# Kernel optimization log

Hardware: AMD Instinct MI355X
Metric: run time of the kernel (lower is better)

The kernel has to match this reference:

```python
import jax, jax.numpy as jnp
import numpy as np

D_MODEL = 1024
HEADS = 16
DILATION = 4
LN_EPS = 1e-5


def setup_inputs() -> dict:
    key = jax.random.key(0)
    ks = jax.random.split(key, 11)
    B, S, D = 2, 4096, D_MODEL
    x = jax.random.normal(ks[0], (B, S, D), dtype=jnp.float32)
    def lin(k):
        kw, kb = jax.random.split(k)
        W = jax.random.normal(kw, (D, D), dtype=jnp.float32) * 0.02  # torch Linear layout [out, in]
        b = jax.random.normal(kb, (D,), dtype=jnp.float32) * 0.02
        return W, b
    Wq, bq = lin(ks[1])
    Wk, bk = lin(ks[2])
    Wv, bv = lin(ks[3])
    Wf, bf = lin(ks[4])
    gamma = jnp.ones((D,), dtype=jnp.float32)
    beta = jnp.zeros((D,), dtype=jnp.float32)
    return {"x": x, "Wq": Wq, "bq": bq, "Wk": Wk, "bk": bk,
            "Wv": Wv, "bv": bv, "Wf": Wf, "bf": bf,
            "gamma": gamma, "beta": beta}


def _layer_norm(x, gamma, beta):
    mu = jnp.mean(x, axis=-1, keepdims=True)
    var = jnp.mean(jnp.square(x - mu), axis=-1, keepdims=True)
    return (x - mu) * jax.lax.rsqrt(var + LN_EPS) * gamma + beta


def reference(x, Wq, bq, Wk, bk, Wv, bv, Wf, bf, gamma, beta):
    B, S, D = x.shape
    dil, H = DILATION, HEADS
    dh = D // H
    pad = (-S) % dil  # padding_size
    xp = jnp.pad(x, ((0, 0), (0, pad), (0, 0)))
    Sp = S + pad
    L = Sp // dil
    # strided (atrous) regrouping: [B, Sp, D] -> [B*dil, L, D]
    xr = xp.reshape(B, L, dil, D).transpose(0, 2, 1, 3).reshape(B * dil, L, D)
    q = xr @ Wq.T + bq
    k = xr @ Wk.T + bk
    v = xr @ Wv.T + bv
    # split heads: [B*dil, H, L, dh]
    q = q.reshape(B * dil, L, H, dh).transpose(0, 2, 1, 3)
    k = k.reshape(B * dil, L, H, dh).transpose(0, 2, 1, 3)
    v = v.reshape(B * dil, L, H, dh).transpose(0, 2, 1, 3)
    scores = jnp.einsum('bhqd,bhkd->bhqk', q, k) / jnp.sqrt(jnp.float32(dh))
    probs = jax.nn.softmax(scores, axis=-1)
    ctx = jnp.einsum('bhqk,bhkd->bhqd', probs, v)
    # merge heads and undo atrous regrouping
    ctx = ctx.transpose(0, 2, 1, 3).reshape(B * dil, L, D)
    ctx = ctx.reshape(B, dil, L, D).transpose(0, 2, 1, 3).reshape(B, Sp, D)
    ctx = ctx[:, :S]
    atted = ctx @ Wf.T + bf  # dropout p=0.0
    final = _layer_norm(atted + x, gamma, beta)
    return (final, atted)
```

## Files before the change

### kernel.cpp

```cpp
#include <hip/hip_runtime.h>
#include <cstdint>
#include <cstddef>

constexpr int B_  = 2;
constexpr int S_  = 4096;
constexpr int D_  = 1024;
constexpr int H_  = 16;
constexpr int DH_ = 64;
constexpr int DIL = 4;
constexpr int L_  = S_ / DIL;
constexpr int M_  = B_ * S_;

typedef __attribute__((ext_vector_type(8))) short short8;
typedef __attribute__((ext_vector_type(4))) float f32x4;

__device__ __forceinline__ unsigned short f2b(float f) {
    union { float f; unsigned u; } v;
    v.f = f;
    unsigned r = v.u + 0x7fff + ((v.u >> 16) & 1);
    return (unsigned short)(r >> 16);
}

#define GLOAD16(gptr, lptr)                                                    \
    __builtin_amdgcn_global_load_lds(                                          \
        (const __attribute__((address_space(1))) void*)(gptr),                 \
        (__attribute__((address_space(3))) void*)(lptr), 16, 0, 0)

__global__ __launch_bounds__(256)
void conv_f2b(const float* __restrict__ in, unsigned short* __restrict__ out, int n4) {
    int i = blockIdx.x * 256 + threadIdx.x;
    if (i < n4) {
        float4 v = reinterpret_cast<const float4*>(in)[i];
        ushort4 o;
        o.x = f2b(v.x); o.y = f2b(v.y); o.z = f2b(v.z); o.w = f2b(v.w);
        reinterpret_cast<ushort4*>(out)[i] = o;
    }
}

template <int OUT_BF16>
__global__ __launch_bounds__(256)
void gemm_mfma(const unsigned short* __restrict__ A,
               const unsigned short* __restrict__ W,
               const float* __restrict__ bias,
               void* __restrict__ Cout, int M, int N, int K) {
    __shared__ unsigned short As[128 * 64];
    __shared__ unsigned short Bs[128 * 64];

    const int tid  = threadIdx.x;
    const int lane = tid & 63, wave = tid >> 6;
    const int l15 = lane & 15, l4 = lane >> 4;
    const int wr = wave >> 1, wc = wave & 1;
    const int bm = blockIdx.y * 128, bn = blockIdx.x * 128;

    f32x4 acc[4][4] = {};

    for (int k0 = 0; k0 < K; k0 += 64) {
        #pragma unroll
        for (int i = 0; i < 4; ++i) {
            int ch = i * 256 + wave * 64 + lane;
            int r = ch >> 3, c8 = ch & 7;
            const unsigned short* ga = A + (size_t)(bm + r) * K + k0 + c8 * 8;
            GLOAD16(ga, (char*)As + (size_t)(i * 256 + wave * 64) * 16);
            const unsigned short* gb = W + (size_t)(bn + r) * K + k0 + c8 * 8;
            GLOAD16(gb, (char*)Bs + (size_t)(i * 256 + wave * 64) * 16);
        }
        __syncthreads();

        #pragma unroll
        for (int ks = 0; ks < 2; ++ks) {
            short8 af[4], bf[4];
            #pragma unroll
            for (int mi = 0; mi < 4; ++mi)
                af[mi] = *reinterpret_cast<const short8*>(
                    &As[(wr * 64 + mi * 16 + l15) * 64 + ks * 32 + l4 * 8]);
            #pragma unroll
            for (int ni = 0; ni < 4; ++ni)
                bf[ni] = *reinterpret_cast<const short8*>(
                    &Bs[(wc * 64 + ni * 16 + l15) * 64 + ks * 32 + l4 * 8]);
            #pragma unroll
            for (int mi = 0; mi < 4; ++mi)
                #pragma unroll
                for (int ni = 0; ni < 4; ++ni)
                    acc[mi][ni] = __builtin_amdgcn_mfma_f32_16x16x32_bf16(
                        af[mi], bf[ni], acc[mi][ni], 0, 0, 0);
        }
        __syncthreads();
    }

    #pragma unroll
    for (int ni = 0; ni < 4; ++ni) {
        int col = bn + wc * 64 + ni * 16 + l15;
        float bv = bias[col];
        #pragma unroll
        for (int mi = 0; mi < 4; ++mi) {
            #pragma unroll
            for (int r = 0; r < 4; ++r) {
                int row = bm + wr * 64 + mi * 16 + l4 * 4 + r;
                float v = acc[mi][ni][r] + bv;
                if (OUT_BF16)
                    ((unsigned short*)Cout)[(size_t)row * N + col] = f2b(v);
                else
                    ((float*)Cout)[(size_t)row * N + col] = v;
            }
        }
    }
}

__global__ __launch_bounds__(256)
void gemm_qkv(const unsigned short* __restrict__ A,
              const unsigned short* __restrict__ W,
              const float* __restrict__ bq, const float* __restrict__ bk,
              const float* __restrict__ bv,
              unsigned short* __restrict__ Qb, unsigned short* __restrict__ Kb,
              unsigned short* __restrict__ Vb, int M, int K) {
    __shared__ unsigned short As[128 * 64];
    __shared__ unsigned short Bs[128 * 64];

    const int tid  = threadIdx.x;
    const int lane = tid & 63, wave = tid >> 6;
    const int l15 = lane & 15, l4 = lane >> 4;
    const int wr = wave >> 1, wc = wave & 1;
    const int bm = blockIdx.y * 128, bn = blockIdx.x * 128;

    f32x4 acc[4][4] = {};

    for (int k0 = 0; k0 < K; k0 += 64) {
        #pragma unroll
        for (int i = 0; i < 4; ++i) {
            int ch = i * 256 + wave * 64 + lane;
            int r = ch >> 3, c8 = ch & 7;
            const unsigned short* ga = A + (size_t)(bm + r) * K + k0 + c8 * 8;
            GLOAD16(ga, (char*)As + (size_t)(i * 256 + wave * 64) * 16);
            const unsigned short* gb = W + (size_t)(bn + r) * K + k0 + c8 * 8;
            GLOAD16(gb, (char*)Bs + (size_t)(i * 256 + wave * 64) * 16);
        }
        __syncthreads();

        #pragma unroll
        for (int ks = 0; ks < 2; ++ks) {
            short8 af[4], bf[4];
            #pragma unroll
            for (int mi = 0; mi < 4; ++mi)
                af[mi] = *reinterpret_cast<const short8*>(
                    &As[(wr * 64 + mi * 16 + l15) * 64 + ks * 32 + l4 * 8]);
            #pragma unroll
            for (int ni = 0; ni < 4; ++ni)
                bf[ni] = *reinterpret_cast<const short8*>(
                    &Bs[(wc * 64 + ni * 16 + l15) * 64 + ks * 32 + l4 * 8]);
            #pragma unroll
            for (int mi = 0; mi < 4; ++mi)
                #pragma unroll
                for (int ni = 0; ni < 4; ++ni)
                    acc[mi][ni] = __builtin_amdgcn_mfma_f32_16x16x32_bf16(
                        af[mi], bf[ni], acc[mi][ni], 0, 0, 0);
        }
        __syncthreads();
    }

    const int seg = bn >> 10;
    const float* bp = (seg == 0) ? bq : (seg == 1) ? bk : bv;
    unsigned short* ob = (seg == 0) ? Qb : (seg == 1) ? Kb : Vb;
    const int cb = bn & 1023;

    #pragma unroll
    for (int ni = 0; ni < 4; ++ni) {
        int col = cb + wc * 64 + ni * 16 + l15;
        float bvv = bp[col];
        #pragma unroll
        for (int mi = 0; mi < 4; ++mi) {
            #pragma unroll
            for (int r = 0; r < 4; ++r) {
                int row = bm + wr * 64 + mi * 16 + l4 * 4 + r;
                ob[(size_t)row * 1024 + col] = f2b(acc[mi][ni][r] + bvv);
            }
        }
    }
}

__global__ __launch_bounds__(256)
void attn_mfma(const unsigned short* __restrict__ Q,
               const unsigned short* __restrict__ K,
               const unsigned short* __restrict__ V,
               unsigned short* __restrict__ O) {
    __shared__ unsigned short Ks[2][64 * 64];
    __shared__ unsigned short Vt[2][64 * 64];

    const int tid = threadIdx.x;
    const int lane = tid & 63, wave = tid >> 6;
    const int l15 = lane & 15, l4 = lane >> 4;
    const int blk = blockIdx.x;
    const int qt = blk & 15;
    const int h  = (blk >> 4) & 15;
    const int bd = blk >> 8;
    const int b = bd >> 2, dd = bd & 3;
    const size_t rowbase = (size_t)b * S_;
    const int colbase = h * DH_;

    short8 qf[2];
    {
        int q = qt * 64 + wave * 16 + l15;
        const unsigned short* qp =
            Q + (rowbase + (size_t)q * DIL + dd) * D_ + colbase;
        qf[0] = *reinterpret_cast<const short8*>(qp + l4 * 8);
        qf[1] = *reinterpret_cast<const short8*>(qp + 32 + l4 * 8);
    }

    auto stageK = [&](int kt, int buf) {
        #pragma unroll
        for (int i = 0; i < 2; ++i) {
            int key = i * 32 + wave * 8 + (lane >> 3);
            int srcc = (lane & 7) ^ (lane >> 3);
            const unsigned short* g =
                K + (rowbase + (size_t)(kt * 64 + key) * DIL + dd) * D_ + colbase + srcc * 8;
            GLOAD16(g, (char*)&Ks[buf][0] + (size_t)(i * 256 + wave * 64) * 16);
        }
    };
    auto loadV = [&](int kt, int i) {
        int c8 = wave * 2 + i;
        return *reinterpret_cast<const short8*>(
            V + (rowbase + (size_t)(kt * 64 + lane) * DIL + dd) * D_ + colbase + c8 * 8);
    };
    auto writeV = [&](int buf, short8 va, short8 vb) {
        #pragma unroll
        for (int i = 0; i < 2; ++i) {
            short8 v = i ? vb : va;
            int c8 = wave * 2 + i;
            #pragma unroll
            for (int j = 0; j < 8; ++j)
                Vt[buf][(c8 * 8 + j) * 64 + (((lane >> 3) ^ j) * 8) + (lane & 7)] =
                    (unsigned short)v[j];
        }
    };

    f32x4 oT[4] = {};
    float m_run = -1e30f, l_run = 0.f;

    stageK(0, 0);
    {
        short8 va = loadV(0, 0), vb = loadV(0, 1);
        writeV(0, va, vb);
    }
    __syncthreads();

    const int srcA = ((l4 & 1) * 2) * 16 + l15;
    const int srcB = srcA + 16;
    const bool hi = (l4 & 2) != 0;

    for (int kt = 0; kt < L_ / 64; ++kt) {
        int cur = kt & 1, nxt = cur ^ 1;
        short8 va, vb;
        if (kt < L_ / 64 - 1) {
            stageK(kt + 1, nxt);
            va = loadV(kt + 1, 0);
            vb = loadV(kt + 1, 1);
        }

        f32x4 sT[4];
        #pragma unroll
        for (int n = 0; n < 4; ++n) {
            int row = n * 16 + l15;
            short8 kf0 = *reinterpret_cast<const short8*>(
                &Ks[cur][row * 64 + ((0 * 4 + l4) ^ (l15 & 7)) * 8]);
            short8 kf1 = *reinterpret_cast<const short8*>(
                &Ks[cur][row * 64 + ((1 * 4 + l4) ^ (l15 & 7)) * 8]);
            f32x4 z = {0.f, 0.f, 0.f, 0.f};
            z = __builtin_amdgcn_mfma_f32_16x16x32_bf16(kf0, qf[0], z, 0, 0, 0);
            z = __builtin_amdgcn_mfma_f32_16x16x32_bf16(kf1, qf[1], z, 0, 0, 0);
            sT[n] = z * 0.125f;
        }

        float mx = -1e30f;
        #pragma unroll
        for (int n = 0; n < 4; ++n)
            #pragma unroll
            for (int r = 0; r < 4; ++r) mx = fmaxf(mx, sT[n][r]);
        mx = fmaxf(mx, __shfl_xor(mx, 16));
        mx = fmaxf(mx, __shfl_xor(mx, 32));
        float m_new = fmaxf(m_run, mx);
        float scale = __expf(m_run - m_new);
        float p[4][4], rsum = 0.f;
        #pragma unroll
        for (int n = 0; n < 4; ++n)
            #pragma unroll
            for (int r = 0; r < 4; ++r) {
                p[n][r] = __expf(sT[n][r] - m_new);
                rsum += p[n][r];
            }
        rsum += __shfl_xor(rsum, 16);
        rsum += __shfl_xor(rsum, 32);
        l_run = l_run * scale + rsum;
        m_run = m_new;
        #pragma unroll
        for (int nd = 0; nd < 4; ++nd) oT[nd] *= scale;

        unsigned pk[4][2];
        #pragma unroll
        for (int n = 0; n < 4; ++n) {
            pk[n][0] = (unsigned)f2b(p[n][0]) | ((unsigned)f2b(p[n][1]) << 16);
            pk[n][1] = (unsigned)f2b(p[n][2]) | ((unsigned)f2b(p[n][3]) << 16);
        }
        unsigned exA[4][2], exB[4][2];
        #pragma unroll
        for (int n = 0; n < 4; ++n) {
            #pragma unroll
            for (int d = 0; d < 2; ++d) {
                exA[n][d] = (unsigned)__shfl((int)pk[n][d], srcA);
                exB[n][d] = (unsigned)__shfl((int)pk[n][d], srcB);
            }
        }

        #pragma unroll
        for (int ks = 0; ks < 2; ++ks) {
            union { uint4 u; short8 s; } pf;
            pf.u.x = hi ? exA[ks * 2 + 1][0] : exA[ks * 2][0];
            pf.u.y = hi ? exA[ks * 2 + 1][1] : exA[ks * 2][1];
            pf.u.z = hi ? exB[ks * 2 + 1][0] : exB[ks * 2][0];
            pf.u.w = hi ? exB[ks * 2 + 1][1] : exB[ks * 2][1];
            #pragma unroll
            for (int nd = 0; nd < 4; ++nd) {
                int row = nd * 16 + l15;
                short8 vf = *reinterpret_cast<const short8*>(
                    &Vt[cur][row * 64 + ((ks * 4 + l4) ^ (l15 & 7)) * 8]);
                oT[nd] = __builtin_amdgcn_mfma_f32_16x16x32_bf16(vf, pf.s, oT[nd], 0, 0, 0);
            }
        }

        if (kt < L_ / 64 - 1) writeV(nxt, va, vb);
        __syncthreads();
    }

    unsigned short* Es = &Ks[0][0];
    float inv = 1.f / l_run;
    #pragma unroll
    for (int nd = 0; nd < 4; ++nd) {
        unsigned lo = (unsigned)f2b(oT[nd][0] * inv) | ((unsigned)f2b(oT[nd][1] * inv) << 16);
        unsigned hiw = (unsigned)f2b(oT[nd][2] * inv) | ((unsigned)f2b(oT[nd][3] * inv) << 16);
        int chunk = nd * 2 + (l4 >> 1);
        int pc = chunk ^ (l15 & 7);
        uint2 w = make_uint2(lo, hiw);
        *reinterpret_cast<uint2*>(&Es[wave * 1024 + l15 * 64 + pc * 8 + (l4 & 1) * 4]) = w;
    }
    __syncthreads();
    {
        int row = lane >> 2;
        int q = qt * 64 + wave * 16 + row;
        unsigned short* op = O + (rowbase + (size_t)q * DIL + dd) * D_ + colbase;
        #pragma unroll
        for (int i = 0; i < 2; ++i) {
            int c = (lane & 3) * 2 + i;
            int pc = c ^ (row & 7);
            uint4 val = *reinterpret_cast<const uint4*>(&Es[wave * 1024 + row * 64 + pc * 8]);
            *reinterpret_cast<uint4*>(op + c * 8) = val;
        }
    }
}

__global__ __launch_bounds__(256)
void add_ln(const float* __restrict__ atted, const float* __restrict__ x,
            const float* __restrict__ gamma, const float* __restrict__ beta,
            float* __restrict__ out) {
    __shared__ float red[8];
    const int tid = threadIdx.x;
    const size_t base = (size_t)blockIdx.x * D_;

    float4 a  = *reinterpret_cast<const float4*>(atted + base + tid * 4);
    float4 xv = *reinterpret_cast<const float4*>(x + base + tid * 4);
    float v0 = a.x + xv.x, v1 = a.y + xv.y, v2 = a.z + xv.z, v3 = a.w + xv.w;

    float s = v0 + v1 + v2 + v3;
    #pragma unroll
    for (int o = 1; o < 64; o <<= 1) s += __shfl_xor(s, o);
    if ((tid & 63) == 0) red[tid >> 6] = s;
    __syncthreads();
    float mean = (red[0] + red[1] + red[2] + red[3]) * (1.0f / D_);

    float d0 = v0 - mean, d1 = v1 - mean, d2 = v2 - mean, d3 = v3 - mean;
    float sq = d0 * d0 + d1 * d1 + d2 * d2 + d3 * d3;
    #pragma unroll
    for (int o = 1; o < 64; o <<= 1) sq += __shfl_xor(sq, o);
    if ((tid & 63) == 0) red[4 + (tid >> 6)] = sq;
    __syncthreads();
    float var = (red[4] + red[5] + red[6] + red[7]) * (1.0f / D_);
    float inv = rsqrtf(var + 1e-5f);

    float4 g  = *reinterpret_cast<const float4*>(gamma + tid * 4);
    float4 bb = *reinterpret_cast<const float4*>(beta + tid * 4);
    float4 o4;
    o4.x = d0 * inv * g.x + bb.x;
    o4.y = d1 * inv * g.y + bb.y;
    o4.z = d2 * inv * g.z + bb.z;
    o4.w = d3 * inv * g.w + bb.w;
    *reinterpret_cast<float4*>(out + base + tid * 4) = o4;
}

extern "C" void kernel_launch(void* const* d_in, const int* in_sizes, int n_in,
                              void* d_out, int out_size, void* d_ws, size_t ws_size,
                              hipStream_t stream) {
    const float* x     = (const float*)d_in[0];
    const float* Wq    = (const float*)d_in[1];
    const float* bq    = (const float*)d_in[2];
    const float* Wk    = (const float*)d_in[3];
    const float* bk    = (const float*)d_in[4];
    const float* Wv    = (const float*)d_in[5];
    const float* bv    = (const float*)d_in[6];
    const float* Wf    = (const float*)d_in[7];
    const float* bf    = (const float*)d_in[8];
    const float* gamma = (const float*)d_in[9];
    const float* beta  = (const float*)d_in[10];

    float* final_out = (float*)d_out;
    float* atted     = final_out + (size_t)M_ * D_;

    unsigned short* xb  = (unsigned short*)d_ws;
    unsigned short* Wqb = xb  + (size_t)M_ * D_;
    unsigned short* Wkb = Wqb + (size_t)D_ * D_;
    unsigned short* Wvb = Wkb + (size_t)D_ * D_;
    unsigned short* Wfb = Wvb + (size_t)D_ * D_;
    unsigned short* Qb  = Wfb + (size_t)D_ * D_;
    unsigned short* Kb  = Qb  + (size_t)M_ * D_;
    unsigned short* Vb  = Kb  + (size_t)M_ * D_;
    unsigned short* ctxb = xb;

    conv_f2b<<<dim3(M_ * D_ / 4 / 256), 256, 0, stream>>>(x,  xb,  M_ * D_ / 4);
    conv_f2b<<<dim3(D_ * D_ / 4 / 256), 256, 0, stream>>>(Wq, Wqb, D_ * D_ / 4);
    conv_f2b<<<dim3(D_ * D_ / 4 / 256), 256, 0, stream>>>(Wk, Wkb, D_ * D_ / 4);
    conv_f2b<<<dim3(D_ * D_ / 4 / 256), 256, 0, stream>>>(Wv, Wvb, D_ * D_ / 4);
    conv_f2b<<<dim3(D_ * D_ / 4 / 256), 256, 0, stream>>>(Wf, Wfb, D_ * D_ / 4);

    gemm_qkv<<<dim3(3072 / 128, M_ / 128), 256, 0, stream>>>(
        xb, Wqb, bq, bk, bv, Qb, Kb, Vb, M_, D_);

    attn_mfma<<<dim3(DIL * B_ * H_ * (L_ / 64)), 256, 0, stream>>>(Qb, Kb, Vb, ctxb);

    gemm_mfma<0><<<dim3(D_ / 128, M_ / 128), 256, 0, stream>>>(
        ctxb, Wfb, bf, atted, M_, D_, D_);

    add_ln<<<dim3(M_), 256, 0, stream>>>(atted, x, gamma, beta, final_out);
}
```

Before: 338.1 us.

## Pre-transpose V, stage via LDS DMA, XCD swizzle grids, fuse weight converts

After: 322.5 us. 1.05x faster.

```diff
diff --git a/kernel.cpp b/kernel.cpp
--- a/kernel.cpp
+++ b/kernel.cpp
@@ -1,4 +1,5 @@
 #include <hip/hip_runtime.h>
+#include <hip/hip_bf16.h>
 #include <cstdint>
 #include <cstddef>
 
@@ -21,6 +22,19 @@
     return (unsigned short)(r >> 16);
 }
 
+__device__ __forceinline__ unsigned pkbf(float a, float b) {
+    float2 t; t.x = a; t.y = b;
+    __hip_bfloat162 h = __float22bfloat162_rn(t);
+    union { __hip_bfloat162 h; unsigned u; } c; c.h = h;
+    return c.u;
+}
+
+__device__ __forceinline__ int xcd_swz(int orig, int nwg) {
+    int q = nwg >> 3, r = nwg & 7;
+    int xcd = orig & 7, idx = orig >> 3;
+    return (xcd < r ? xcd * (q + 1) : r * (q + 1) + (xcd - r) * q) + idx;
+}
+
 #define GLOAD16(gptr, lptr)                                                    \
     __builtin_amdgcn_global_load_lds(                                          \
         (const __attribute__((address_space(1))) void*)(gptr),                 \
@@ -37,6 +51,20 @@
     }
 }
 
+__global__ __launch_bounds__(256)
+void conv_w4(const float* __restrict__ w0, const float* __restrict__ w1,
+             const float* __restrict__ w2, const float* __restrict__ w3,
+             unsigned short* __restrict__ out) {
+    int bid = blockIdx.x;
+    int which = bid >> 10;
+    const float* src = (which == 0) ? w0 : (which == 1) ? w1 : (which == 2) ? w2 : w3;
+    int i = (bid & 1023) * 256 + threadIdx.x;
+    float4 v = reinterpret_cast<const float4*>(src)[i];
+    ushort4 o;
+    o.x = f2b(v.x); o.y = f2b(v.y); o.z = f2b(v.z); o.w = f2b(v.w);
+    reinterpret_cast<ushort4*>(out + (size_t)which * D_ * D_)[i] = o;
+}
+
 template <int OUT_BF16>
 __global__ __launch_bounds__(256)
 void gemm_mfma(const unsigned short* __restrict__ A,
@@ -50,7 +78,9 @@
     const int lane = tid & 63, wave = tid >> 6;
     const int l15 = lane & 15, l4 = lane >> 4;
     const int wr = wave >> 1, wc = wave & 1;
-    const int bm = blockIdx.y * 128, bn = blockIdx.x * 128;
+    const int gy = M >> 7;
+    const int wg = xcd_swz(blockIdx.x, gridDim.x);
+    const int bm = (wg % gy) * 128, bn = (wg / gy) * 128;
 
     f32x4 acc[4][4] = {};
 
@@ -120,7 +150,9 @@
     const int lane = tid & 63, wave = tid >> 6;
     const int l15 = lane & 15, l4 = lane >> 4;
     const int wr = wave >> 1, wc = wave & 1;
-    const int bm = blockIdx.y * 128, bn = blockIdx.x * 128;
+    const int gy = M >> 7;
+    const int wg = xcd_swz(blockIdx.x, gridDim.x);
+    const int bm = (wg % gy) * 128, bn = (wg / gy) * 128;
 
     f32x4 acc[4][4] = {};
 
@@ -178,17 +210,53 @@
 }
 
 __global__ __launch_bounds__(256)
+void tvt(const unsigned short* __restrict__ Vb, unsigned short* __restrict__ Vtg) {
+    __shared__ unsigned short Ts[64 * 64];
+    const int tid = threadIdx.x;
+    const int blk = blockIdx.x;
+    const int lt = blk & 15;
+    const int h  = (blk >> 4) & 15;
+    const int bd = blk >> 8;
+    const int b = bd >> 2, dd = bd & 3;
+    const size_t rowbase = (size_t)b * S_;
+
+    #pragma unroll
+    for (int i = 0; i < 2; ++i) {
+        int ch = i * 256 + tid;
+        int lloc = ch >> 3, c8 = ch & 7;
+        short8 v = *reinterpret_cast<const short8*>(
+            Vb + (rowbase + (size_t)(lt * 64 + lloc) * DIL + dd) * D_ + h * 64 + c8 * 8);
+        #pragma unroll
+        for (int j = 0; j < 8; ++j) {
+            int dh = c8 * 8 + j;
+            Ts[dh * 64 + (((lloc >> 3) ^ (dh & 7)) * 8) + (lloc & 7)] = (unsigned short)v[j];
+        }
+    }
+    __syncthreads();
+
+    const size_t obase = ((size_t)(bd * 16 + h) * 64) * L_;
+    #pragma unroll
+    for (int i = 0; i < 2; ++i) {
+        int ch = i * 256 + tid;
+        int dh = ch >> 3, c = ch & 7;
+        uint4 val = *reinterpret_cast<const uint4*>(&Ts[dh * 64 + ((c ^ (dh & 7)) * 8)]);
+        *reinterpret_cast<uint4*>(Vtg + obase + (size_t)dh * L_ + lt * 64 + c * 8) = val;
+    }
+}
+
+__global__ __launch_bounds__(256)
 void attn_mfma(const unsigned short* __restrict__ Q,
                const unsigned short* __restrict__ K,
-               const unsigned short* __restrict__ V,
+               const unsigned short* __restrict__ Vtg,
                unsigned short* __restrict__ O) {
     __shared__ unsigned short Ks[2][64 * 64];
-    __shared__ unsigned short Vt[2][64 * 64];
+    __shared__ unsigned short Vs[2][64 * 64];
+    __shared__ unsigned short Ps[4][1024];
 
     const int tid = threadIdx.x;
     const int lane = tid & 63, wave = tid >> 6;
     const int l15 = lane & 15, l4 = lane >> 4;
-    const int blk = blockIdx.x;
+    const int blk = xcd_swz(blockIdx.x, gridDim.x);
     const int qt = blk & 15;
     const int h  = (blk >> 4) & 15;
     const int bd = blk >> 8;
@@ -205,6 +273,8 @@
         qf[1] = *reinterpret_cast<const short8*>(qp + 32 + l4 * 8);
     }
 
+    const unsigned short* vbase = Vtg + ((size_t)(bd * 16 + h) * 64) * L_;
+
     auto stageK = [&](int kt, int buf) {
         #pragma unroll
         for (int i = 0; i < 2; ++i) {
@@ -215,20 +285,13 @@
             GLOAD16(g, (char*)&Ks[buf][0] + (size_t)(i * 256 + wave * 64) * 16);
         }
     };
-    auto loadV = [&](int kt, int i) {
-        int c8 = wave * 2 + i;
-        return *reinterpret_cast<const short8*>(
-            V + (rowbase + (size_t)(kt * 64 + lane) * DIL + dd) * D_ + colbase + c8 * 8);
-    };
-    auto writeV = [&](int buf, short8 va, short8 vb) {
+    auto stageV = [&](int kt, int buf) {
         #pragma unroll
         for (int i = 0; i < 2; ++i) {
-            short8 v = i ? vb : va;
-            int c8 = wave * 2 + i;
-            #pragma unroll
-            for (int j = 0; j < 8; ++j)
-                Vt[buf][(c8 * 8 + j) * 64 + (((lane >> 3) ^ j) * 8) + (lane & 7)] =
-                    (unsigned short)v[j];
+            int dh = i * 32 + wave * 8 + (lane >> 3);
+            int srcc = (lane & 7) ^ (lane >> 3);
+            const unsigned short* g = vbase + (size_t)dh * L_ + kt * 64 + srcc * 8;
+            GLOAD16(g, (char*)&Vs[buf][0] + (size_t)(i * 256 + wave * 64) * 16);
         }
     };
 
@@ -236,23 +299,15 @@
     float m_run = -1e30f, l_run = 0.f;
 
     stageK(0, 0);
-    {
-        short8 va = loadV(0, 0), vb = loadV(0, 1);
-        writeV(0, va, vb);
-    }
+    stageV(0, 0);
     __syncthreads();
 
-    const int srcA = ((l4 & 1) * 2) * 16 + l15;
-    const int srcB = srcA + 16;
-    const bool hi = (l4 & 2) != 0;
-
-    for (int kt = 0; kt < L_ / 64; ++kt) {
+    constexpr int NT = L_ / 64;
+    for (int kt = 0; kt < NT; ++kt) {
         int cur = kt & 1, nxt = cur ^ 1;
-        short8 va, vb;
-        if (kt < L_ / 64 - 1) {
+        if (kt < NT - 1) {
             stageK(kt + 1, nxt);
-            va = loadV(kt + 1, 0);
-            vb = loadV(kt + 1, 1);
+            stageV(kt + 1, nxt);
         }
 
         f32x4 sT[4];
@@ -293,51 +348,43 @@
         #pragma unroll
         for (int nd = 0; nd < 4; ++nd) oT[nd] *= scale;
 
-        unsigned pk[4][2];
         #pragma unroll
         for (int n = 0; n < 4; ++n) {
-            pk[n][0] = (unsigned)f2b(p[n][0]) | ((unsigned)f2b(p[n][1]) << 16);
-            pk[n][1] = (unsigned)f2b(p[n][2]) | ((unsigned)f2b(p[n][3]) << 16);
-        }
-        unsigned exA[4][2], exB[4][2];
-        #pragma unroll
-        for (int n = 0; n < 4; ++n) {
-            #pragma unroll
-            for (int d = 0; d < 2; ++d) {
-                exA[n][d] = (unsigned)__shfl((int)pk[n][d], srcA);
-                exB[n][d] = (unsigned)__shfl((int)pk[n][d], srcB);
+            uint2 w;
+            w.x = pkbf(p[n][0], p[n][1]);
+            w.y = pkbf(p[n][2], p[n][3]);
+            int c = n * 2 + (l4 >> 1);
+            int pc = c ^ (l15 & 7);
+            *reinterpret_cast<uint2*>(&Ps[wave][l15 * 64 + pc * 8 + (l4 & 1) * 4]) = w;
+        }
+        short8 pb0 = *reinterpret_cast<const short8*>(
+            &Ps[wave][l15 * 64 + ((0 * 4 + l4) ^ (l15 & 7)) * 8]);
+        short8 pb1 = *reinterpret_cast<const short8*>(
+            &Ps[wave][l15 * 64 + ((1 * 4 + l4) ^ (l15 & 7)) * 8]);
+
+        #pragma unroll
+        for (int ks = 0; ks < 2; ++ks) {
+            short8 pb = ks ? pb1 : pb0;
+            #pragma unroll
+            for (int nd = 0; nd < 4; ++nd) {
+                short8 vf = *reinterpret_cast<const short8*>(
+                    &Vs[cur][(nd * 16 + l15) * 64 + ((ks * 4 + l4) ^ (l15 & 7)) * 8]);
+                oT[nd] = __builtin_amdgcn_mfma_f32_16x16x32_bf16(vf, pb, oT[nd], 0, 0, 0);
             }
         }
 
-        #pragma unroll
-        for (int ks = 0; ks < 2; ++ks) {
-            union { uint4 u; short8 s; } pf;
-            pf.u.x = hi ? exA[ks * 2 + 1][0] : exA[ks * 2][0];
-            pf.u.y = hi ? exA[ks * 2 + 1][1] : exA[ks * 2][1];
-            pf.u.z = hi ? exB[ks * 2 + 1][0] : exB[ks * 2][0];
-            pf.u.w = hi ? exB[ks * 2 + 1][1] : exB[ks * 2][1];
-            #pragma unroll
-            for (int nd = 0; nd < 4; ++nd) {
-                int row = nd * 16 + l15;
-                short8 vf = *reinterpret_cast<const short8*>(
-                    &Vt[cur][row * 64 + ((ks * 4 + l4) ^ (l15 & 7)) * 8]);
-                oT[nd] = __builtin_amdgcn_mfma_f32_16x16x32_bf16(vf, pf.s, oT[nd], 0, 0, 0);
-            }
-        }
-
-        if (kt < L_ / 64 - 1) writeV(nxt, va, vb);
         __syncthreads();
     }
 
-    unsigned short* Es = &Ks[0][0];
+    unsigned short* Es = &Ps[0][0];
     float inv = 1.f / l_run;
     #pragma unroll
     for (int nd = 0; nd < 4; ++nd) {
-        unsigned lo = (unsigned)f2b(oT[nd][0] * inv) | ((unsigned)f2b(oT[nd][1] * inv) << 16);
-        unsigned hiw = (unsigned)f2b(oT[nd][2] * inv) | ((unsigned)f2b(oT[nd][3] * inv) << 16);
+        uint2 w;
+        w.x = pkbf(oT[nd][0] * inv, oT[nd][1] * inv);
+        w.y = pkbf(oT[nd][2] * inv, oT[nd][3] * inv);
         int chunk = nd * 2 + (l4 >> 1);
         int pc = chunk ^ (l15 & 7);
-        uint2 w = make_uint2(lo, hiw);
         *reinterpret_cast<uint2*>(&Es[wave * 1024 + l15 * 64 + pc * 8 + (l4 & 1) * 4]) = w;
     }
     __syncthreads();
@@ -419,20 +466,20 @@
     unsigned short* Qb  = Wfb + (size_t)D_ * D_;
     unsigned short* Kb  = Qb  + (size_t)M_ * D_;
     unsigned short* Vb  = Kb  + (size_t)M_ * D_;
+    unsigned short* Vtg = Vb  + (size_t)M_ * D_;
     unsigned short* ctxb = xb;
 
-    conv_f2b<<<dim3(M_ * D_ / 4 / 256), 256, 0, stream>>>(x,  xb,  M_ * D_ / 4);
-    conv_f2b<<<dim3(D_ * D_ / 4 / 256), 256, 0, stream>>>(Wq, Wqb, D_ * D_ / 4);
-    conv_f2b<<<dim3(D_ * D_ / 4 / 256), 256, 0, stream>>>(Wk, Wkb, D_ * D_ / 4);
-    conv_f2b<<<dim3(D_ * D_ / 4 / 256), 256, 0, stream>>>(Wv, Wvb, D_ * D_ / 4);
-    conv_f2b<<<dim3(D_ * D_ / 4 / 256), 256, 0, stream>>>(Wf, Wfb, D_ * D_ / 4);
-
-    gemm_qkv<<<dim3(3072 / 128, M_ / 128), 256, 0, stream>>>(
+    conv_f2b<<<dim3(M_ * D_ / 4 / 256), 256, 0, stream>>>(x, xb, M_ * D_ / 4);
+    conv_w4<<<dim3(4096), 256, 0, stream>>>(Wq, Wk, Wv, Wf, Wqb);
+
+    gemm_qkv<<<dim3((3072 / 128) * (M_ / 128)), 256, 0, stream>>>(
         xb, Wqb, bq, bk, bv, Qb, Kb, Vb, M_, D_);
 
-    attn_mfma<<<dim3(DIL * B_ * H_ * (L_ / 64)), 256, 0, stream>>>(Qb, Kb, Vb, ctxb);
-
-    gemm_mfma<0><<<dim3(D_ / 128, M_ / 128), 256, 0, stream>>>(
+    tvt<<<dim3(DIL * B_ * H_ * (L_ / 64)), 256, 0, stream>>>(Vb, Vtg);
+
+    attn_mfma<<<dim3(DIL * B_ * H_ * (L_ / 64)), 256, 0, stream>>>(Qb, Kb, Vtg, ctxb);
+
+    gemm_mfma<0><<<dim3((D_ / 128) * (M_ / 128)), 256, 0, stream>>>(
         ctxb, Wfb, bf, atted, M_, D_, D_);
 
     add_ln<<<dim3(M_), 256, 0, stream>>>(atted, x, gamma, beta, final_out);
```
